# Kernel tuning notes

Hardware: AMD Instinct MI355X
Metric: run time of the kernel (lower is better)

## Reference

```python
import jax, jax.numpy as jnp
import numpy as np

N = 8192
D_IN = 128
D_OUT = 64


def setup_inputs() -> dict:
    key = jax.random.key(0)
    k1, k2, k3 = jax.random.split(key, 3)
    features = jax.random.normal(k1, (N, D_IN), dtype=jnp.float32)
    # uniform [0,1) entries -> strictly positive row sums (degrees)
    adjacency_matrix = jax.random.uniform(k2, (N, N), dtype=jnp.float32)
    weight = jax.random.normal(k3, (D_IN, D_OUT), dtype=jnp.float32)
    return {"features": features, "adjacency_matrix": adjacency_matrix, "weight": weight}


def reference(features, adjacency_matrix, weight):
    # degree_matrix = diag(rowsum(A)); inverse(sqrt(diag(d))) == diag(d^{-1/2})
    deg = jnp.sum(adjacency_matrix, axis=1)            # [N]
    d_inv_sqrt = 1.0 / jnp.sqrt(deg)                   # [N]
    # D^{-1/2} A D^{-1/2} via broadcasting instead of dense diag matmuls
    norm_adj = d_inv_sqrt[:, None] * adjacency_matrix * d_inv_sqrt[None, :]  # [N,N]
    # (norm_adj @ X) @ W -- contract small dim last for efficiency
    h = norm_adj @ features                            # [N, D_IN]
    return jax.nn.relu(h @ weight)                     # [N, D_OUT]
```

## Files before the change

kernel.cpp:

```cpp
#include <hip/hip_runtime.h>

#define N_NODES 8192
#define D_IN    128
#define D_OUT   64
#define NSPLIT  8

typedef __attribute__((ext_vector_type(8))) short short8;
typedef __attribute__((ext_vector_type(4))) float f32x4;

__device__ __forceinline__ short f2bf(float f) {
    unsigned u = __builtin_bit_cast(unsigned, f);
    u += 0x7fff + ((u >> 16) & 1);
    return (short)(u >> 16);
}

__global__ __launch_bounds__(256) void k_deg(const float* __restrict__ A,
                                             float* __restrict__ dis) {
    const int wave = threadIdx.x >> 6;
    const int lane = threadIdx.x & 63;
    const int row  = blockIdx.x * 4 + wave;
    const float4* Ar = (const float4*)(A + (size_t)row * N_NODES);
    float s = 0.f;
#pragma unroll
    for (int i = 0; i < 32; ++i) {
        float4 v = Ar[lane + 64 * i];
        s += (v.x + v.y) + (v.z + v.w);
    }
#pragma unroll
    for (int off = 32; off; off >>= 1) s += __shfl_down(s, off, 64);
    if (lane == 0) dis[row] = rsqrtf(s);
}

__global__ __launch_bounds__(256) void k_gpack(const float* __restrict__ X,
                                               const float* __restrict__ W,
                                               const float* __restrict__ dis,
                                               unsigned short* __restrict__ Gp) {
    __shared__ float Wl[D_IN * D_OUT];
    __shared__ float Xl[32 * 129];
    const int t = blockIdx.x, tid = threadIdx.x;

    const float4* W4 = (const float4*)W;
    float4* Wl4 = (float4*)Wl;
#pragma unroll
    for (int i = 0; i < 8; ++i) Wl4[tid + 256 * i] = W4[tid + 256 * i];
    const float4* X4 = (const float4*)(X + (size_t)t * 32 * D_IN);
#pragma unroll
    for (int i = 0; i < 4; ++i) {
        int idx = tid + 256 * i;
        float4 v = X4[idx];
        int r = idx >> 5, c = (idx & 31) * 4;
        float* dst = Xl + r * 129 + c;
        dst[0] = v.x; dst[1] = v.y; dst[2] = v.z; dst[3] = v.w;
    }
    __syncthreads();

    const int kl = tid & 31;
    const int nb = (tid >> 5) * 8;
    float acc[8] = {0.f, 0.f, 0.f, 0.f, 0.f, 0.f, 0.f, 0.f};
    const float* xr = Xl + kl * 129;
    for (int d = 0; d < D_IN; ++d) {
        float xv = xr[d];
        const float* wr = Wl + d * D_OUT + nb;
#pragma unroll
        for (int c = 0; c < 8; ++c) acc[c] += xv * wr[c];
    }
    const float scale = dis[t * 32 + kl];
    const int quad = kl >> 3, j = kl & 7;
#pragma unroll
    for (int c = 0; c < 8; ++c) {
        int n = nb + c;
        int u = n >> 4;
        int lanei = quad * 16 + (n & 15);
        Gp[(((size_t)t * 4 + u) * 64 + lanei) * 8 + j] = (unsigned short)f2bf(acc[c] * scale);
    }
}

__global__ __launch_bounds__(256) void k_spmm(const float* __restrict__ A,
                                              const unsigned short* __restrict__ Gp,
                                              float* __restrict__ h2s) {
    const int lane = threadIdx.x & 63;
    const int wave = threadIdx.x >> 6;
    const int quad = lane >> 4;
    const int l15  = lane & 15;
    const int row  = blockIdx.x * 64 + wave * 16 + l15;
    const float* Ar = A + (size_t)row * N_NODES;
    const int kt0 = blockIdx.y * 32;

    f32x4 acc[4] = {};
    const short8* Gq = (const short8*)Gp;

    for (int kt = kt0; kt < kt0 + 32; ++kt) {
        const float4* pa = (const float4*)(Ar + kt * 32 + quad * 8);
        float4 a0 = pa[0], a1 = pa[1];
        short8 af;
        af[0] = f2bf(a0.x); af[1] = f2bf(a0.y); af[2] = f2bf(a0.z); af[3] = f2bf(a0.w);
        af[4] = f2bf(a1.x); af[5] = f2bf(a1.y); af[6] = f2bf(a1.z); af[7] = f2bf(a1.w);
        const short8* gb = Gq + (size_t)kt * 4 * 64 + lane;
#pragma unroll
        for (int u = 0; u < 4; ++u) {
            short8 bf = gb[u * 64];
            acc[u] = __builtin_amdgcn_mfma_f32_16x16x32_bf16(af, bf, acc[u], 0, 0, 0);
        }
    }
    float* H = h2s + (size_t)blockIdx.y * ((size_t)N_NODES * D_OUT);
    const int r0 = blockIdx.x * 64 + wave * 16 + quad * 4;
#pragma unroll
    for (int u = 0; u < 4; ++u) {
#pragma unroll
        for (int r = 0; r < 4; ++r) {
            H[(size_t)(r0 + r) * D_OUT + u * 16 + l15] = acc[u][r];
        }
    }
}

__global__ __launch_bounds__(256) void k_out(const float* __restrict__ h2s,
                                             const float* __restrict__ dis,
                                             float* __restrict__ out) {
    const int idx = blockIdx.x * 256 + threadIdx.x;
    const f32x4* H = (const f32x4*)h2s;
    const int slice = N_NODES * D_OUT / 4;
    f32x4 s = H[idx];
#pragma unroll
    for (int p = 1; p < NSPLIT; ++p) s += H[idx + (size_t)p * slice];
    const float sc = dis[idx >> 4];
    f32x4 o;
#pragma unroll
    for (int c = 0; c < 4; ++c) o[c] = fmaxf(s[c] * sc, 0.f);
    ((f32x4*)out)[idx] = o;
}

extern "C" void kernel_launch(void* const* d_in, const int* in_sizes, int n_in,
                              void* d_out, int out_size, void* d_ws, size_t ws_size,
                              hipStream_t stream) {
    const float* X = (const float*)d_in[0];
    const float* A = (const float*)d_in[1];
    const float* W = (const float*)d_in[2];
    float* out = (float*)d_out;

    char* ws = (char*)d_ws;
    float*          dis = (float*)ws;
    unsigned short* Gp  = (unsigned short*)(ws + 32768);
    float*          h2s = (float*)(ws + 32768 + 1048576);

    k_deg  <<<N_NODES / 4, 256, 0, stream>>>(A, dis);
    k_gpack<<<N_NODES / 32, 256, 0, stream>>>(X, W, dis, Gp);
    k_spmm <<<dim3(N_NODES / 64, NSPLIT), 256, 0, stream>>>(A, Gp, h2s);
    k_out  <<<(N_NODES * D_OUT / 4) / 256, 256, 0, stream>>>(h2s, dis, out);
}
```

Before: 423.4 us.

## Fuse degree pass with bf16 MFMA-layout packing of adjacency, then stream packed A

The degree kernel now also converts A to bf16 and writes it in the exact per-lane MFMA fragment layout, using nontemporal loads with software prefetch. The SpMM kernel then reads the compact 128 MB packed copy with fully contiguous per-lane loads and no in-loop conversion, instead of re-reading the 256 MB fp32 matrix. The rsqrt moves into the consumers, which now read raw degrees. The new path needs a large extra workspace; if the workspace is too small it falls back to the original kernels. Total bytes moved stay similar, since the pack adds a 128 MB write, so any gain depends on better access patterns and on the packed copy possibly staying resident in cache.

```diff
diff --git a/kernel.cpp b/kernel.cpp
--- a/kernel.cpp
+++ b/kernel.cpp
@@ -14,26 +14,74 @@
     return (short)(u >> 16);
 }
 
-__global__ __launch_bounds__(256) void k_deg(const float* __restrict__ A,
-                                             float* __restrict__ dis) {
+__global__ __launch_bounds__(256) void k_degpack(const float* __restrict__ A,
+                                                 float* __restrict__ deg,
+                                                 unsigned short* __restrict__ Ap) {
+    const int tid = threadIdx.x;
+    const int r = tid >> 4, c = tid & 15;
+    const int ri = blockIdx.x;
+    const int row = ri * 16 + r;
+    const f32x4* Ar = (const f32x4*)(A + (size_t)row * N_NODES + c * 8);
+    short8* Apv = (short8*)Ap;
+    const size_t ubase = ((size_t)ri * 256 + (c >> 2)) * 64 + (c & 3) * 16 + r;
+
+    float s = 0.f;
+    f32x4 a0 = __builtin_nontemporal_load(Ar);
+    f32x4 a1 = __builtin_nontemporal_load(Ar + 1);
+#pragma unroll 4
+    for (int m = 0; m < 64; ++m) {
+        f32x4 b0, b1;
+        if (m < 63) {
+            b0 = __builtin_nontemporal_load(Ar + (m + 1) * 32);
+            b1 = __builtin_nontemporal_load(Ar + (m + 1) * 32 + 1);
+        }
+        s += (a0[0] + a0[1]) + (a0[2] + a0[3]) + (a1[0] + a1[1]) + (a1[2] + a1[3]);
+        short8 p;
+        p[0] = f2bf(a0[0]); p[1] = f2bf(a0[1]); p[2] = f2bf(a0[2]); p[3] = f2bf(a0[3]);
+        p[4] = f2bf(a1[0]); p[5] = f2bf(a1[1]); p[6] = f2bf(a1[2]); p[7] = f2bf(a1[3]);
+        Apv[ubase + (size_t)m * 256] = p;
+        a0 = b0; a1 = b1;
+    }
+#pragma unroll
+    for (int off = 1; off < 16; off <<= 1) s += __shfl_xor(s, off, 64);
+    if (c == 0) deg[row] = s;
+}
+
+__global__ __launch_bounds__(256) void k_spmm_bf16(const unsigned short* __restrict__ Ap,
+                                                   const unsigned short* __restrict__ Gp,
+                                                   float* __restrict__ h2s) {
+    const int lane = threadIdx.x & 63;
     const int wave = threadIdx.x >> 6;
-    const int lane = threadIdx.x & 63;
-    const int row  = blockIdx.x * 4 + wave;
-    const float4* Ar = (const float4*)(A + (size_t)row * N_NODES);
-    float s = 0.f;
-#pragma unroll
+    const int quad = lane >> 4;
+    const int l15  = lane & 15;
+    const int ri   = blockIdx.x * 4 + wave;
+    const int kt0  = blockIdx.y * 32;
+
+    const short8* Af = (const short8*)Ap + ((size_t)ri * 256 + kt0) * 64 + lane;
+    const short8* Gq = (const short8*)Gp + (size_t)kt0 * 256 + lane;
+
+    f32x4 acc[4] = {};
+#pragma unroll 2
     for (int i = 0; i < 32; ++i) {
-        float4 v = Ar[lane + 64 * i];
-        s += (v.x + v.y) + (v.z + v.w);
-    }
-#pragma unroll
-    for (int off = 32; off; off >>= 1) s += __shfl_down(s, off, 64);
-    if (lane == 0) dis[row] = rsqrtf(s);
+        short8 af = Af[i * 64];
+        const short8* gb = Gq + i * 256;
+#pragma unroll
+        for (int u = 0; u < 4; ++u) {
+            acc[u] = __builtin_amdgcn_mfma_f32_16x16x32_bf16(af, gb[u * 64], acc[u], 0, 0, 0);
+        }
+    }
+    float* H = h2s + (size_t)blockIdx.y * ((size_t)N_NODES * D_OUT);
+    const int r0 = ri * 16 + quad * 4;
+#pragma unroll
+    for (int u = 0; u < 4; ++u)
+#pragma unroll
+        for (int r = 0; r < 4; ++r)
+            H[(size_t)(r0 + r) * D_OUT + u * 16 + l15] = acc[u][r];
 }
 
 __global__ __launch_bounds__(256) void k_gpack(const float* __restrict__ X,
                                                const float* __restrict__ W,
-                                               const float* __restrict__ dis,
+                                               const float* __restrict__ deg,
                                                unsigned short* __restrict__ Gp) {
     __shared__ float Wl[D_IN * D_OUT];
     __shared__ float Xl[32 * 129];
@@ -64,7 +112,7 @@
 #pragma unroll
         for (int c = 0; c < 8; ++c) acc[c] += xv * wr[c];
     }
-    const float scale = dis[t * 32 + kl];
+    const float scale = rsqrtf(deg[t * 32 + kl]);
     const int quad = kl >> 3, j = kl & 7;
 #pragma unroll
     for (int c = 0; c < 8; ++c) {
@@ -75,9 +123,42 @@
     }
 }
 
-__global__ __launch_bounds__(256) void k_spmm(const float* __restrict__ A,
-                                              const unsigned short* __restrict__ Gp,
-                                              float* __restrict__ h2s) {
+__global__ __launch_bounds__(256) void k_out(const float* __restrict__ h2s,
+                                             const float* __restrict__ deg,
+                                             float* __restrict__ out) {
+    const int idx = blockIdx.x * 256 + threadIdx.x;
+    const f32x4* H = (const f32x4*)h2s;
+    const int slice = N_NODES * D_OUT / 4;
+    f32x4 s = H[idx];
+#pragma unroll
+    for (int p = 1; p < NSPLIT; ++p) s += H[idx + (size_t)p * slice];
+    const float sc = rsqrtf(deg[idx >> 4]);
+    f32x4 o;
+#pragma unroll
+    for (int c = 0; c < 4; ++c) o[c] = fmaxf(s[c] * sc, 0.f);
+    ((f32x4*)out)[idx] = o;
+}
+
+__global__ __launch_bounds__(256) void k_deg(const float* __restrict__ A,
+                                             float* __restrict__ deg) {
+    const int wave = threadIdx.x >> 6;
+    const int lane = threadIdx.x & 63;
+    const int row  = blockIdx.x * 4 + wave;
+    const float4* Ar = (const float4*)(A + (size_t)row * N_NODES);
+    float s = 0.f;
+#pragma unroll
+    for (int i = 0; i < 32; ++i) {
+        float4 v = Ar[lane + 64 * i];
+        s += (v.x + v.y) + (v.z + v.w);
+    }
+#pragma unroll
+    for (int off = 32; off; off >>= 1) s += __shfl_down(s, off, 64);
+    if (lane == 0) deg[row] = s;
+}
+
+__global__ __launch_bounds__(256) void k_spmm_f32(const float* __restrict__ A,
+                                                  const unsigned short* __restrict__ Gp,
+                                                  float* __restrict__ h2s) {
     const int lane = threadIdx.x & 63;
     const int wave = threadIdx.x >> 6;
     const int quad = lane >> 4;
@@ -98,35 +179,16 @@
         const short8* gb = Gq + (size_t)kt * 4 * 64 + lane;
 #pragma unroll
         for (int u = 0; u < 4; ++u) {
-            short8 bf = gb[u * 64];
-            acc[u] = __builtin_amdgcn_mfma_f32_16x16x32_bf16(af, bf, acc[u], 0, 0, 0);
+            acc[u] = __builtin_amdgcn_mfma_f32_16x16x32_bf16(af, gb[u * 64], acc[u], 0, 0, 0);
         }
     }
     float* H = h2s + (size_t)blockIdx.y * ((size_t)N_NODES * D_OUT);
     const int r0 = blockIdx.x * 64 + wave * 16 + quad * 4;
 #pragma unroll
-    for (int u = 0; u < 4; ++u) {
-#pragma unroll
-        for (int r = 0; r < 4; ++r) {
+    for (int u = 0; u < 4; ++u)
+#pragma unroll
+        for (int r = 0; r < 4; ++r)
             H[(size_t)(r0 + r) * D_OUT + u * 16 + l15] = acc[u][r];
-        }
-    }
-}
-
-__global__ __launch_bounds__(256) void k_out(const float* __restrict__ h2s,
-                                             const float* __restrict__ dis,
-                                             float* __restrict__ out) {
-    const int idx = blockIdx.x * 256 + threadIdx.x;
-    const f32x4* H = (const f32x4*)h2s;
-    const int slice = N_NODES * D_OUT / 4;
-    f32x4 s = H[idx];
-#pragma unroll
-    for (int p = 1; p < NSPLIT; ++p) s += H[idx + (size_t)p * slice];
-    const float sc = dis[idx >> 4];
-    f32x4 o;
-#pragma unroll
-    for (int c = 0; c < 4; ++c) o[c] = fmaxf(s[c] * sc, 0.f);
-    ((f32x4*)out)[idx] = o;
 }
 
 extern "C" void kernel_launch(void* const* d_in, const int* in_sizes, int n_in,
@@ -138,12 +200,22 @@
     float* out = (float*)d_out;
 
     char* ws = (char*)d_ws;
-    float*          dis = (float*)ws;
+    float*          deg = (float*)ws;
     unsigned short* Gp  = (unsigned short*)(ws + 32768);
     float*          h2s = (float*)(ws + 32768 + 1048576);
-
-    k_deg  <<<N_NODES / 4, 256, 0, stream>>>(A, dis);
-    k_gpack<<<N_NODES / 32, 256, 0, stream>>>(X, W, dis, Gp);
-    k_spmm <<<dim3(N_NODES / 64, NSPLIT), 256, 0, stream>>>(A, Gp, h2s);
-    k_out  <<<(N_NODES * D_OUT / 4) / 256, 256, 0, stream>>>(h2s, dis, out);
-}
+    unsigned short* Ap  = (unsigned short*)(ws + 32768 + 1048576 + 16777216);
+
+    const size_t need = 32768 + 1048576 + 16777216 + (size_t)N_NODES * N_NODES * 2;
+
+    if (ws_size >= need) {
+        k_degpack<<<N_NODES / 16, 256, 0, stream>>>(A, deg, Ap);
+        k_gpack  <<<N_NODES / 32, 256, 0, stream>>>(X, W, deg, Gp);
+        k_spmm_bf16<<<dim3(N_NODES / 64, NSPLIT), 256, 0, stream>>>(Ap, Gp, h2s);
+        k_out    <<<(N_NODES * D_OUT / 4) / 256, 256, 0, stream>>>(h2s, deg, out);
+    } else {
+        k_deg    <<<N_NODES / 4, 256, 0, stream>>>(A, deg);
+        k_gpack  <<<N_NODES / 32, 256, 0, stream>>>(X, W, deg, Gp);
+        k_spmm_f32<<<dim3(N_NODES / 64, NSPLIT), 256, 0, stream>>>(A, Gp, h2s);
+        k_out    <<<(N_NODES * D_OUT / 4) / 256, 256, 0, stream>>>(h2s, deg, out);
+    }
+}
```

Result: faster. 411.0 us (-2.9%).
